# Optimization experiments

Hardware: AMD Instinct MI355X
Metric: run time of the kernel (lower is better)

Reference implementation:

```python
import jax, jax.numpy as jnp
import numpy as np

N, K, D, E = 20000, 63, 50, 300  # nodes, neighbors per node, hidden dim, entity input dim


def setup_inputs() -> dict:
    key = jax.random.key(0)
    ks = jax.random.split(key, 12)
    inp = {
        "query_emb": jax.random.normal(ks[0], (N, D), jnp.float32),
        "entity_emb": jax.random.normal(ks[1], (N, E), jnp.float32),
        "neighbor_embs": jax.random.normal(ks[2], (N, K, D), jnp.float32),
        "neighbor_scores": jax.random.uniform(ks[3], (N, K + 1), jnp.float32),
        # learned parameters (xavier-ish scale)
        "Wp": jax.random.normal(ks[4], (D, E), jnp.float32) * (1.0 / np.sqrt(E)),
        "bp": jnp.zeros((D,), jnp.float32),
        "Wbil": jax.random.normal(ks[5], (D, D, D), jnp.float32) * (1.0 / D),
        "bbil": jnp.zeros((D,), jnp.float32),
        "Wg": jax.random.normal(ks[6], (D, D), jnp.float32) * (1.0 / np.sqrt(D)),
        "g_bias": jnp.zeros((D,), jnp.float32),
        "Wr": jax.random.normal(ks[7], (1, D), jnp.float32) * (1.0 / np.sqrt(D)),
        "br": jnp.zeros((1,), jnp.float32),
    }
    return inp


def reference(query_emb, entity_emb, neighbor_embs, neighbor_scores,
              Wp, bp, Wbil, bbil, Wg, g_bias, Wr, br):
    # entity projection: [N,E] -> [N,D]
    ent = entity_emb @ Wp.T + bp
    # bilinear query-entity interaction: node[n,o] = q[n,i] Wbil[o,i,j] ent[n,j] + bbil[o]
    node = jnp.einsum('ni,oij,nj->no', query_emb, Wbil, ent) + bbil  # [N,D]
    # ragged neighbor texts = K paraembeds + the node's own embedding (uniform K here)
    texts = jnp.concatenate([neighbor_embs, node[:, None, :]], axis=1)  # [N,K+1,D]
    # GRN: project neighbors, scale by attention scores, sum over neighbors
    # (dropout p=0.01 is identity in eval mode)
    proj = jnp.einsum('nkd,od->nko', texts, Wg)           # [N,K+1,D]
    agg = jnp.einsum('nko,nk->no', proj, neighbor_scores)  # attention-weighted scatter-sum
    feats = jax.nn.elu(agg + g_bias)                       # bias + ELU activation
    # rank score head: [N,D] -> [N,1]
    return feats @ Wr.T + br
```

## Files before the change

kernel.cpp:

```cpp
#include <hip/hip_runtime.h>
#include <math.h>

#define NN 20000
typedef unsigned int uint;
typedef unsigned short ushort;
typedef __attribute__((ext_vector_type(8))) short bf16x8;
typedef __attribute__((ext_vector_type(4))) float f32x4;

__device__ __forceinline__ ushort f2b(float x) {
    uint u = __float_as_uint(x);
    return (ushort)((u + 0x7FFFu + ((u >> 16) & 1u)) >> 16);
}
__device__ __forceinline__ float b2f(ushort b) {
    return __uint_as_float(((uint)b) << 16);
}

__global__ __launch_bounds__(256) void kPrep(const float* __restrict__ Wbil,
                                             const float* __restrict__ Wp,
                                             ushort* __restrict__ WtT,
                                             ushort* __restrict__ WpB) {
    const int stride = gridDim.x * 256;
    for (int i = blockIdx.x * 256 + threadIdx.x; i < 64 * 2560; i += stride) {
        int o = i / 2560, k = i - o * 2560;
        WtT[i] = (o < 50 && k < 2500) ? f2b(Wbil[o * 2500 + k]) : (ushort)0;
    }
    for (int i = blockIdx.x * 256 + threadIdx.x; i < 64 * 384; i += stride) {
        int d = i / 384, e = i - d * 384;
        WpB[i] = (d < 50 && e < 300) ? f2b(Wp[d * 300 + e]) : (ushort)0;
    }
}

__global__ __launch_bounds__(256) void kMain(
    const float* __restrict__ q,
    const float* __restrict__ entity,
    const float* __restrict__ bp,
    const ushort* __restrict__ WpB,
    const ushort* __restrict__ WtT,
    float* __restrict__ part)
{
    __shared__ ushort qs[64 * 50];
    __shared__ ushort es[64 * 50];
    __shared__ ushort Xs[64 * 136];
    __shared__ ushort Bs[64 * 136];

    const int tid = threadIdx.x;
    const int h = blockIdx.x & 1;
    const int n0 = (blockIdx.x >> 1) * 64;
    const int w = tid >> 6, lane = tid & 63;
    const int c = lane & 15, quad = lane >> 4;
    const int nl = tid >> 2;
    const int kc = (tid & 3) * 32;

    for (int i = tid; i < 3200; i += 256) {
        int r = i / 50, d = i - r * 50;
        float v = (n0 + r < NN) ? q[(size_t)(n0 + r) * 50 + d] : 0.f;
        qs[i] = f2b(v);
    }

    f32x4 accE[4] = {{0.f,0.f,0.f,0.f},{0.f,0.f,0.f,0.f},{0.f,0.f,0.f,0.f},{0.f,0.f,0.f,0.f}};
    for (int t = 0; t < 3; ++t) {
        const int e0 = t * 128;
        __syncthreads();
        {
            const int node = n0 + nl;
            uint pk[16];
            #pragma unroll
            for (int u8 = 0; u8 < 8; ++u8) {
                const int e = e0 + kc + u8 * 4;
                float4 v = make_float4(0.f, 0.f, 0.f, 0.f);
                if (node < NN) {
                    if (e + 3 < 300) v = *(const float4*)(entity + (size_t)node * 300 + e);
                    else {
                        if (e < 300)     v.x = entity[(size_t)node * 300 + e];
                        if (e + 1 < 300) v.y = entity[(size_t)node * 300 + e + 1];
                        if (e + 2 < 300) v.z = entity[(size_t)node * 300 + e + 2];
                    }
                }
                pk[u8 * 2]     = (uint)f2b(v.x) | ((uint)f2b(v.y) << 16);
                pk[u8 * 2 + 1] = (uint)f2b(v.z) | ((uint)f2b(v.w) << 16);
            }
            uint4* dst = (uint4*)(Xs + nl * 136 + kc);
            #pragma unroll
            for (int m = 0; m < 4; ++m)
                dst[m] = make_uint4(pk[m*4], pk[m*4+1], pk[m*4+2], pk[m*4+3]);
        }
        {
            const uint4* src = (const uint4*)(WpB + nl * 384 + e0 + kc);
            uint4 v0 = src[0], v1 = src[1], v2 = src[2], v3 = src[3];
            uint4* dst = (uint4*)(Bs + nl * 136 + kc);
            dst[0] = v0; dst[1] = v1; dst[2] = v2; dst[3] = v3;
        }
        __syncthreads();
        #pragma unroll
        for (int ks = 0; ks < 4; ++ks) {
            bf16x8 a = *(const bf16x8*)(Xs + (w * 16 + c) * 136 + ks * 32 + quad * 8);
            #pragma unroll
            for (int nt = 0; nt < 4; ++nt) {
                bf16x8 b = *(const bf16x8*)(Bs + (nt * 16 + c) * 136 + ks * 32 + quad * 8);
                accE[nt] = __builtin_amdgcn_mfma_f32_16x16x32_bf16(a, b, accE[nt], 0, 0, 0);
            }
        }
    }
    #pragma unroll
    for (int nt = 0; nt < 4; ++nt) {
        const int d = nt * 16 + c;
        if (d < 50) {
            const float bpd = bp[d];
            #pragma unroll
            for (int r = 0; r < 4; ++r) {
                const int node = w * 16 + quad * 4 + r;
                es[node * 50 + d] = f2b(accE[nt][r] + bpd);
            }
        }
    }

    f32x4 acc[4] = {{0.f,0.f,0.f,0.f},{0.f,0.f,0.f,0.f},{0.f,0.f,0.f,0.f},{0.f,0.f,0.f,0.f}};
    const int kb0 = h * 1280;
    for (int t = 0; t < 10; ++t) {
        const int kbase = kb0 + t * 128;
        __syncthreads();
        {
            const uint4* src = (const uint4*)(WtT + nl * 2560 + kbase + kc);
            uint4 v0 = src[0], v1 = src[1], v2 = src[2], v3 = src[3];
            uint4* dst = (uint4*)(Bs + nl * 136 + kc);
            dst[0] = v0; dst[1] = v1; dst[2] = v2; dst[3] = v3;
        }
        {
            int kg = kbase + kc;
            int i = kg / 50, j = kg - i * 50;
            const ushort* qsr = qs + nl * 50;
            const ushort* esr = es + nl * 50;
            float qv = b2f(qsr[i < 49 ? i : 49]);
            uint pk[16];
            #pragma unroll
            for (int u2 = 0; u2 < 16; ++u2) {
                ushort lo = f2b(qv * b2f(esr[j]));
                if (++j == 50) { j = 0; ++i; qv = b2f(qsr[i < 49 ? i : 49]); }
                ushort hi = f2b(qv * b2f(esr[j]));
                if (++j == 50) { j = 0; ++i; qv = b2f(qsr[i < 49 ? i : 49]); }
                pk[u2] = (uint)lo | ((uint)hi << 16);
            }
            uint4* dst = (uint4*)(Xs + nl * 136 + kc);
            #pragma unroll
            for (int m = 0; m < 4; ++m)
                dst[m] = make_uint4(pk[m*4], pk[m*4+1], pk[m*4+2], pk[m*4+3]);
        }
        __syncthreads();
        #pragma unroll
        for (int ks = 0; ks < 4; ++ks) {
            bf16x8 a = *(const bf16x8*)(Xs + (w * 16 + c) * 136 + ks * 32 + quad * 8);
            #pragma unroll
            for (int nt = 0; nt < 4; ++nt) {
                bf16x8 b = *(const bf16x8*)(Bs + (nt * 16 + c) * 136 + ks * 32 + quad * 8);
                acc[nt] = __builtin_amdgcn_mfma_f32_16x16x32_bf16(a, b, acc[nt], 0, 0, 0);
            }
        }
    }
    #pragma unroll
    for (int nt = 0; nt < 4; ++nt) {
        const int o = nt * 16 + c;
        #pragma unroll
        for (int r = 0; r < 4; ++r) {
            const int node = n0 + w * 16 + quad * 4 + r;
            if (node < NN)
                part[((size_t)h * NN + node) * 64 + o] = acc[nt][r];
        }
    }
}

__global__ __launch_bounds__(256) void kB(const float* __restrict__ nb,
                                          const float* __restrict__ scores,
                                          const float* __restrict__ part,
                                          const float* __restrict__ bbil,
                                          const float* __restrict__ Wg,
                                          const float* __restrict__ g_bias,
                                          const float* __restrict__ Wr,
                                          const float* __restrict__ br,
                                          float* __restrict__ out) {
    __shared__ float Wgs[50 * 51];
    __shared__ float scs[256];
    __shared__ float tv[4][52];

    const int tid = threadIdx.x;
    const int n0 = blockIdx.x * 4;
    for (int idx = tid; idx < 2500; idx += 256) {
        int o = idx / 50, d = idx - o * 50;
        Wgs[o * 51 + d] = Wg[idx];
    }
    scs[tid] = scores[(size_t)n0 * 64 + tid];
    __syncthreads();

    const int w = tid >> 6, lane = tid & 63;
    const int n = n0 + w;
    if (lane < 25) {
        const int d2 = lane * 2;
        const float* base = nb + (size_t)n * 3150 + d2;
        const float* sw = &scs[w * 64];
        float t0 = 0.f, t1 = 0.f;
        #pragma unroll 9
        for (int k = 0; k < 63; ++k) {
            const float2 v = *(const float2*)(base + k * 50);
            t0 += sw[k] * v.x; t1 += sw[k] * v.y;
        }
        const float2 p0 = *(const float2*)(part + (size_t)n * 64 + d2);
        const float2 p1 = *(const float2*)(part + ((size_t)NN + n) * 64 + d2);
        tv[w][d2]     = t0 + sw[63] * (p0.x + p1.x + bbil[d2]);
        tv[w][d2 + 1] = t1 + sw[63] * (p0.y + p1.y + bbil[d2 + 1]);
    }
    __syncthreads();

    float p = 0.f;
    if (lane < 50) {
        float a = g_bias[lane];
        const float* wrow = &Wgs[lane * 51];
        const float* twv = &tv[w][0];
        #pragma unroll 10
        for (int d = 0; d < 50; ++d) a += wrow[d] * twv[d];
        const float f = a > 0.f ? a : (__expf(a) - 1.f);
        p = f * Wr[lane];
    }
    #pragma unroll
    for (int off = 32; off; off >>= 1) p += __shfl_down(p, off);
    if (lane == 0) out[n] = p + br[0];
}

extern "C" void kernel_launch(void* const* d_in, const int* in_sizes, int n_in,
                              void* d_out, int out_size, void* d_ws, size_t ws_size,
                              hipStream_t stream) {
    const float* q_   = (const float*)d_in[0];
    const float* ent  = (const float*)d_in[1];
    const float* nb   = (const float*)d_in[2];
    const float* scr  = (const float*)d_in[3];
    const float* Wp   = (const float*)d_in[4];
    const float* bp   = (const float*)d_in[5];
    const float* Wb   = (const float*)d_in[6];
    const float* bb   = (const float*)d_in[7];
    const float* Wg   = (const float*)d_in[8];
    const float* gb   = (const float*)d_in[9];
    const float* Wr   = (const float*)d_in[10];
    const float* br   = (const float*)d_in[11];
    float* out = (float*)d_out;

    ushort* WtT = (ushort*)d_ws;
    ushort* WpB = WtT + 64 * 2560;
    float*  part = (float*)(WpB + 64 * 384);

    hipLaunchKernelGGL(kPrep, dim3(184),  dim3(256), 0, stream, Wb, Wp, WtT, WpB);
    hipLaunchKernelGGL(kMain, dim3(626),  dim3(256), 0, stream, q_, ent, bp, WpB, WtT, part);
    hipLaunchKernelGGL(kB,    dim3(5000), dim3(256), 0, stream, nb, scr, part, bb, Wg, gb, Wr, br, out);
}
```

Measured before the change: 454.7 us.

## Pad bilinear weight to 64-wide j blocks and build A fragments in registers

Measured after the change: 438.0 us. 3.7% less time.

```diff
diff --git a/kernel.cpp b/kernel.cpp
--- a/kernel.cpp
+++ b/kernel.cpp
@@ -7,6 +7,8 @@
 typedef __attribute__((ext_vector_type(8))) short bf16x8;
 typedef __attribute__((ext_vector_type(4))) float f32x4;
 
+union U8 { uint4 u; bf16x8 v; };
+
 __device__ __forceinline__ ushort f2b(float x) {
     uint u = __float_as_uint(x);
     return (ushort)((u + 0x7FFFu + ((u >> 16) & 1u)) >> 16);
@@ -14,34 +16,41 @@
 __device__ __forceinline__ float b2f(ushort b) {
     return __uint_as_float(((uint)b) << 16);
 }
+__device__ __forceinline__ uint pkmul(uint e2, float qv) {
+    float lo = __uint_as_float(e2 << 16) * qv;
+    float hi = __uint_as_float(e2 & 0xFFFF0000u) * qv;
+    uint ul = (__float_as_uint(lo) + 0x8000u) >> 16;
+    uint uh = (__float_as_uint(hi) + 0x8000u) & 0xFFFF0000u;
+    return ul | uh;
+}
 
 __global__ __launch_bounds__(256) void kPrep(const float* __restrict__ Wbil,
                                              const float* __restrict__ Wp,
-                                             ushort* __restrict__ WtT,
+                                             ushort* __restrict__ WtT2,
                                              ushort* __restrict__ WpB) {
     const int stride = gridDim.x * 256;
-    for (int i = blockIdx.x * 256 + threadIdx.x; i < 64 * 2560; i += stride) {
-        int o = i / 2560, k = i - o * 2560;
-        WtT[i] = (o < 50 && k < 2500) ? f2b(Wbil[o * 2500 + k]) : (ushort)0;
-    }
-    for (int i = blockIdx.x * 256 + threadIdx.x; i < 64 * 384; i += stride) {
-        int d = i / 384, e = i - d * 384;
-        WpB[i] = (d < 50 && e < 300) ? f2b(Wp[d * 300 + e]) : (ushort)0;
-    }
-}
-
-__global__ __launch_bounds__(256) void kMain(
+    for (int idx = blockIdx.x * 256 + threadIdx.x; idx < 64 * 3200; idx += stride) {
+        int o = idx / 3200, k = idx - o * 3200;
+        int i = k >> 6, j = k & 63;
+        WtT2[idx] = (o < 50 && j < 50) ? f2b(Wbil[o * 2500 + i * 50 + j]) : (ushort)0;
+    }
+    for (int idx = blockIdx.x * 256 + threadIdx.x; idx < 64 * 384; idx += stride) {
+        int d = idx / 384, e = idx - d * 384;
+        WpB[idx] = (d < 50 && e < 300) ? f2b(Wp[d * 300 + e]) : (ushort)0;
+    }
+}
+
+__global__ __launch_bounds__(256, 3) void kMain(
     const float* __restrict__ q,
     const float* __restrict__ entity,
     const float* __restrict__ bp,
     const ushort* __restrict__ WpB,
-    const ushort* __restrict__ WtT,
+    const ushort* __restrict__ WtT2,
     float* __restrict__ part)
 {
     __shared__ ushort qs[64 * 50];
-    __shared__ ushort es[64 * 50];
-    __shared__ ushort Xs[64 * 136];
-    __shared__ ushort Bs[64 * 136];
+    __shared__ ushort es[64 * 72];
+    __shared__ ushort Bs[2][64 * 144];
 
     const int tid = threadIdx.x;
     const int h = blockIdx.x & 1;
@@ -50,6 +59,7 @@
     const int c = lane & 15, quad = lane >> 4;
     const int nl = tid >> 2;
     const int kc = (tid & 3) * 32;
+    const int myrow = w * 16 + c;
 
     for (int i = tid; i < 3200; i += 256) {
         int r = i / 50, d = i - r * 50;
@@ -57,6 +67,8 @@
         qs[i] = f2b(v);
     }
 
+    ushort* BsE = &Bs[0][0];
+    ushort* BsW = &Bs[1][0];
     f32x4 accE[4] = {{0.f,0.f,0.f,0.f},{0.f,0.f,0.f,0.f},{0.f,0.f,0.f,0.f},{0.f,0.f,0.f,0.f}};
     for (int t = 0; t < 3; ++t) {
         const int e0 = t * 128;
@@ -68,18 +80,12 @@
             for (int u8 = 0; u8 < 8; ++u8) {
                 const int e = e0 + kc + u8 * 4;
                 float4 v = make_float4(0.f, 0.f, 0.f, 0.f);
-                if (node < NN) {
-                    if (e + 3 < 300) v = *(const float4*)(entity + (size_t)node * 300 + e);
-                    else {
-                        if (e < 300)     v.x = entity[(size_t)node * 300 + e];
-                        if (e + 1 < 300) v.y = entity[(size_t)node * 300 + e + 1];
-                        if (e + 2 < 300) v.z = entity[(size_t)node * 300 + e + 2];
-                    }
-                }
+                if (node < NN && e < 300)
+                    v = *(const float4*)(entity + (size_t)node * 300 + e);
                 pk[u8 * 2]     = (uint)f2b(v.x) | ((uint)f2b(v.y) << 16);
                 pk[u8 * 2 + 1] = (uint)f2b(v.z) | ((uint)f2b(v.w) << 16);
             }
-            uint4* dst = (uint4*)(Xs + nl * 136 + kc);
+            uint4* dst = (uint4*)(BsE + nl * 144 + kc);
             #pragma unroll
             for (int m = 0; m < 4; ++m)
                 dst[m] = make_uint4(pk[m*4], pk[m*4+1], pk[m*4+2], pk[m*4+3]);
@@ -87,16 +93,16 @@
         {
             const uint4* src = (const uint4*)(WpB + nl * 384 + e0 + kc);
             uint4 v0 = src[0], v1 = src[1], v2 = src[2], v3 = src[3];
-            uint4* dst = (uint4*)(Bs + nl * 136 + kc);
+            uint4* dst = (uint4*)(BsW + nl * 144 + kc);
             dst[0] = v0; dst[1] = v1; dst[2] = v2; dst[3] = v3;
         }
         __syncthreads();
         #pragma unroll
         for (int ks = 0; ks < 4; ++ks) {
-            bf16x8 a = *(const bf16x8*)(Xs + (w * 16 + c) * 136 + ks * 32 + quad * 8);
+            bf16x8 a = *(const bf16x8*)(BsE + myrow * 144 + ks * 32 + quad * 8);
             #pragma unroll
             for (int nt = 0; nt < 4; ++nt) {
-                bf16x8 b = *(const bf16x8*)(Bs + (nt * 16 + c) * 136 + ks * 32 + quad * 8);
+                bf16x8 b = *(const bf16x8*)(BsW + (nt * 16 + c) * 144 + ks * 32 + quad * 8);
                 accE[nt] = __builtin_amdgcn_mfma_f32_16x16x32_bf16(a, b, accE[nt], 0, 0, 0);
             }
         }
@@ -104,58 +110,63 @@
     #pragma unroll
     for (int nt = 0; nt < 4; ++nt) {
         const int d = nt * 16 + c;
-        if (d < 50) {
-            const float bpd = bp[d];
-            #pragma unroll
-            for (int r = 0; r < 4; ++r) {
-                const int node = w * 16 + quad * 4 + r;
-                es[node * 50 + d] = f2b(accE[nt][r] + bpd);
+        const float bias = (d < 50) ? bp[d] : 0.f;
+        #pragma unroll
+        for (int r = 0; r < 4; ++r) {
+            const int row = w * 16 + quad * 4 + r;
+            es[row * 72 + d] = (d < 50) ? f2b(accE[nt][r] + bias) : (ushort)0;
+        }
+    }
+    const ushort* myes = es + myrow * 72;
+    const uint4 es0 = *(const uint4*)(myes + quad * 8);
+    const uint4 es1 = *(const uint4*)(myes + 32 + quad * 8);
+    const ushort* qrow = qs + myrow * 50;
+
+    const int kb0 = h ? 1664 : 0;
+    const int ntiles = h ? 12 : 13;
+    f32x4 acc[4] = {{0.f,0.f,0.f,0.f},{0.f,0.f,0.f,0.f},{0.f,0.f,0.f,0.f},{0.f,0.f,0.f,0.f}};
+
+    __syncthreads();
+    {
+        const uint4* src = (const uint4*)(WtT2 + nl * 3200 + kb0 + kc);
+        uint4 v0 = src[0], v1 = src[1], v2 = src[2], v3 = src[3];
+        uint4* dst = (uint4*)(&Bs[0][0] + nl * 144 + kc);
+        dst[0] = v0; dst[1] = v1; dst[2] = v2; dst[3] = v3;
+    }
+    __syncthreads();
+
+    for (int t = 0; t < ntiles; ++t) {
+        uint4 p0, p1, p2, p3;
+        if (t + 1 < ntiles) {
+            const uint4* src = (const uint4*)(WtT2 + nl * 3200 + kb0 + (t + 1) * 128 + kc);
+            p0 = src[0]; p1 = src[1]; p2 = src[2]; p3 = src[3];
+        }
+        const ushort* Bcur = &Bs[t & 1][0];
+        const int i0 = (kb0 >> 6) + 2 * t;
+        #pragma unroll
+        for (int ip = 0; ip < 2; ++ip) {
+            const float qv = b2f(qrow[i0 + ip]);
+            #pragma unroll
+            for (int hf = 0; hf < 2; ++hf) {
+                const uint4 eu = hf ? es1 : es0;
+                U8 ua;
+                ua.u = make_uint4(pkmul(eu.x, qv), pkmul(eu.y, qv),
+                                  pkmul(eu.z, qv), pkmul(eu.w, qv));
+                const int ko = ip * 64 + hf * 32 + quad * 8;
+                #pragma unroll
+                for (int nt = 0; nt < 4; ++nt) {
+                    bf16x8 b = *(const bf16x8*)(Bcur + (nt * 16 + c) * 144 + ko);
+                    acc[nt] = __builtin_amdgcn_mfma_f32_16x16x32_bf16(ua.v, b, acc[nt], 0, 0, 0);
+                }
             }
         }
-    }
-
-    f32x4 acc[4] = {{0.f,0.f,0.f,0.f},{0.f,0.f,0.f,0.f},{0.f,0.f,0.f,0.f},{0.f,0.f,0.f,0.f}};
-    const int kb0 = h * 1280;
-    for (int t = 0; t < 10; ++t) {
-        const int kbase = kb0 + t * 128;
+        if (t + 1 < ntiles) {
+            uint4* dst = (uint4*)(&Bs[(t + 1) & 1][0] + nl * 144 + kc);
+            dst[0] = p0; dst[1] = p1; dst[2] = p2; dst[3] = p3;
+        }
         __syncthreads();
-        {
-            const uint4* src = (const uint4*)(WtT + nl * 2560 + kbase + kc);
-            uint4 v0 = src[0], v1 = src[1], v2 = src[2], v3 = src[3];
-            uint4* dst = (uint4*)(Bs + nl * 136 + kc);
-            dst[0] = v0; dst[1] = v1; dst[2] = v2; dst[3] = v3;
-        }
-        {
-            int kg = kbase + kc;
-            int i = kg / 50, j = kg - i * 50;
-            const ushort* qsr = qs + nl * 50;
-            const ushort* esr = es + nl * 50;
-            float qv = b2f(qsr[i < 49 ? i : 49]);
-            uint pk[16];
-            #pragma unroll
-            for (int u2 = 0; u2 < 16; ++u2) {
-                ushort lo = f2b(qv * b2f(esr[j]));
-                if (++j == 50) { j = 0; ++i; qv = b2f(qsr[i < 49 ? i : 49]); }
-                ushort hi = f2b(qv * b2f(esr[j]));
-                if (++j == 50) { j = 0; ++i; qv = b2f(qsr[i < 49 ? i : 49]); }
-                pk[u2] = (uint)lo | ((uint)hi << 16);
-            }
-            uint4* dst = (uint4*)(Xs + nl * 136 + kc);
-            #pragma unroll
-            for (int m = 0; m < 4; ++m)
-                dst[m] = make_uint4(pk[m*4], pk[m*4+1], pk[m*4+2], pk[m*4+3]);
-        }
-        __syncthreads();
-        #pragma unroll
-        for (int ks = 0; ks < 4; ++ks) {
-            bf16x8 a = *(const bf16x8*)(Xs + (w * 16 + c) * 136 + ks * 32 + quad * 8);
-            #pragma unroll
-            for (int nt = 0; nt < 4; ++nt) {
-                bf16x8 b = *(const bf16x8*)(Bs + (nt * 16 + c) * 136 + ks * 32 + quad * 8);
-                acc[nt] = __builtin_amdgcn_mfma_f32_16x16x32_bf16(a, b, acc[nt], 0, 0, 0);
-            }
-        }
-    }
+    }
+
     #pragma unroll
     for (int nt = 0; nt < 4; ++nt) {
         const int o = nt * 16 + c;
@@ -241,11 +252,11 @@
     const float* br   = (const float*)d_in[11];
     float* out = (float*)d_out;
 
-    ushort* WtT = (ushort*)d_ws;
-    ushort* WpB = WtT + 64 * 2560;
+    ushort* WtT2 = (ushort*)d_ws;
+    ushort* WpB  = WtT2 + 64 * 3200;
     float*  part = (float*)(WpB + 64 * 384);
 
-    hipLaunchKernelGGL(kPrep, dim3(184),  dim3(256), 0, stream, Wb, Wp, WtT, WpB);
-    hipLaunchKernelGGL(kMain, dim3(626),  dim3(256), 0, stream, q_, ent, bp, WpB, WtT, part);
+    hipLaunchKernelGGL(kPrep, dim3(256),  dim3(256), 0, stream, Wb, Wp, WtT2, WpB);
+    hipLaunchKernelGGL(kMain, dim3(626),  dim3(256), 0, stream, q_, ent, bp, WpB, WtT2, part);
     hipLaunchKernelGGL(kB,    dim3(5000), dim3(256), 0, stream, nb, scr, part, bb, Wg, gb, Wr, br, out);
 }
```
